# Kernel tuning notes

Hardware: AMD Instinct MI355X
Metric: run time of the kernel (lower is better)

## Reference

```python
import jax, jax.numpy as jnp
import numpy as np

N_HEAD = 16

def setup_inputs() -> dict:
    key = jax.random.key(0)
    k1, k2, k3 = jax.random.split(key, 3)
    B, T, C = 4, 2048, 1024
    x = jax.random.normal(k1, (B, T, C), dtype=jnp.float32)
    w_attn = jax.random.normal(k2, (C, 3 * C), dtype=jnp.float32) * (1.0 / np.sqrt(C))
    w_proj = jax.random.normal(k3, (C, C), dtype=jnp.float32) * (1.0 / np.sqrt(C))
    return {"x": x, "w_attn": w_attn, "w_proj": w_proj}

def reference(x, w_attn, w_proj):
    B, T, C = x.shape
    H = N_HEAD
    D = C // H
    qkv = x @ w_attn  # [B, T, 3C]
    q, k, v = jnp.split(qkv, 3, axis=2)
    # [B, H, T, D]
    q = q.reshape(B, T, H, D).transpose(0, 2, 1, 3)
    k = k.reshape(B, T, H, D).transpose(0, 2, 1, 3)
    v = v.reshape(B, T, H, D).transpose(0, 2, 1, 3)
    att = jnp.einsum('bhqd,bhkd->bhqk', q, k) * (1.0 / np.sqrt(D))
    causal = jnp.tril(jnp.ones((T, T), dtype=bool))
    att = jnp.where(causal[None, None, :, :], att, -jnp.inf)
    att = jax.nn.softmax(att, axis=-1)
    y = jnp.einsum('bhqk,bhkd->bhqd', att, v)  # [B, H, T, D]
    y = y.transpose(0, 2, 1, 3).reshape(B, T, C)
    return y @ w_proj
```

## Files before the change

kernel.cpp:

```cpp
#include <hip/hip_runtime.h>
#include <hip/hip_bf16.h>
#include <math.h>

#define B_   4
#define T_   2048
#define C_   1024
#define H_   16
#define D_   64
#define M_   (B_*T_)
#define N3   (3*C_)
#define KDIM C_

typedef __attribute__((ext_vector_type(8)))  short bf16x8;
typedef __attribute__((ext_vector_type(4)))  float f32x4;
typedef __attribute__((ext_vector_type(16))) float f32x16;
typedef __attribute__((ext_vector_type(4)))  unsigned int u32x4;

#define MFMA16(a,b,c) __builtin_amdgcn_mfma_f32_16x16x32_bf16(a,b,c,0,0,0)
#define MFMA32(a,b,c) __builtin_amdgcn_mfma_f32_32x32x16_bf16(a,b,c,0,0,0)

#define QSCALE 0.18033688011112042f

__device__ __forceinline__ unsigned short f2bf(float f) {
  union { float f; unsigned u; } a; a.f = f;
  unsigned r = a.u + 0x7fffu + ((a.u >> 16) & 1u);
  return (unsigned short)(r >> 16);
}

__device__ __forceinline__ unsigned cvtpk(float lo, float hi) {
  unsigned r;
  asm("v_cvt_pk_bf16_f32 %0, %1, %2" : "=v"(r) : "v"(lo), "v"(hi));
  return r;
}

__device__ __forceinline__ void gload16(const void* g, void* l) {
  __builtin_amdgcn_global_load_lds(
      (const __attribute__((address_space(1))) void*)g,
      (__attribute__((address_space(3))) void*)l, 16, 0, 0);
}

__global__ void cast_f32_bf16(const float* __restrict__ in,
                              unsigned short* __restrict__ out, int n) {
  int i = (blockIdx.x * 256 + threadIdx.x) * 4;
  if (i >= n) return;
  float4 v = *(const float4*)(in + i);
  ushort4 o;
  o.x = f2bf(v.x); o.y = f2bf(v.y); o.z = f2bf(v.z); o.w = f2bf(v.w);
  *(ushort4*)(out + i) = o;
}

__global__ void transpose_cast(const float* __restrict__ in,
                               unsigned short* __restrict__ out,
                               int R, int Ncols) {
  __shared__ float tile[32][33];
  int bc = blockIdx.x * 32;
  int br = blockIdx.y * 32;
  int tx = threadIdx.x, ty = threadIdx.y;
  #pragma unroll
  for (int i = ty; i < 32; i += 8)
    tile[i][tx] = in[(size_t)(br + i) * Ncols + bc + tx];
  __syncthreads();
  #pragma unroll
  for (int i = ty; i < 32; i += 8)
    out[(size_t)(bc + i) * R + br + tx] = f2bf(tile[tx][i]);
}

template<int MODE>
__global__ __launch_bounds__(256)
void gemm128(const unsigned short* __restrict__ A,
             const unsigned short* __restrict__ Bt,
             unsigned short* __restrict__ qo,
             unsigned short* __restrict__ ko,
             unsigned short* __restrict__ vto,
             float* __restrict__ outf) {
  __shared__ short Asl[128 * 64];
  __shared__ short Bsl[128 * 64];
  const int tid  = threadIdx.x;
  const int wid  = tid >> 6, lane = tid & 63;
  const int l15  = lane & 15, l4 = lane >> 4;
  const int tm   = blockIdx.y * 128;
  const int tn   = blockIdx.x * 128;
  const int wm   = (wid >> 1) * 64, wn = (wid & 1) * 64;

  f32x4 acc[4][4] = {};
  const int stoff = wid * 1024 + lane * 16;

  for (int kt = 0; kt < KDIM; kt += 64) {
    __syncthreads();
    #pragma unroll
    for (int ro = 0; ro < 4; ++ro) {
      int off = ro * 4096 + stoff;
      int row = off >> 7;
      int ce  = (off & 127) >> 1;
      gload16(A  + (size_t)(tm + row) * KDIM + kt + ce,
              (char*)Asl + ro * 4096 + wid * 1024);
      gload16(Bt + (size_t)(tn + row) * KDIM + kt + ce,
              (char*)Bsl + ro * 4096 + wid * 1024);
    }
    __syncthreads();

    #pragma unroll
    for (int ks = 0; ks < 2; ++ks) {
      bf16x8 af[4], bfr[4];
      #pragma unroll
      for (int i = 0; i < 4; ++i) {
        af[i]  = *(const bf16x8*)&Asl[(wm + i*16 + l15) * 64 + ks*32 + l4*8];
        bfr[i] = *(const bf16x8*)&Bsl[(wn + i*16 + l15) * 64 + ks*32 + l4*8];
      }
      #pragma unroll
      for (int mi = 0; mi < 4; ++mi)
        #pragma unroll
        for (int ni = 0; ni < 4; ++ni)
          acc[mi][ni] = MFMA16(af[mi], bfr[ni], acc[mi][ni]);
    }
  }

  #pragma unroll
  for (int mi = 0; mi < 4; ++mi) {
    #pragma unroll
    for (int ni = 0; ni < 4; ++ni) {
      #pragma unroll
      for (int r = 0; r < 4; ++r) {
        int m = tm + wm + mi*16 + l4*4 + r;
        int n = tn + wn + ni*16 + l15;
        float val = acc[mi][ni][r];
        if (MODE == 0) {
          int b = m >> 11, t = m & (T_ - 1);
          int which = n >> 10, n1 = n & (C_ - 1);
          int h = n1 >> 6, d = n1 & 63;
          size_t bh = (size_t)(b * H_ + h);
          if (which == 0)      qo[(bh * T_ + t) * D_ + d] = f2bf(val * QSCALE);
          else if (which == 1) ko[(bh * T_ + t) * D_ + d] = f2bf(val);
          else                 vto[(bh * D_ + d) * T_ + t] = f2bf(val);
        } else {
          outf[(size_t)m * C_ + n] = val;
        }
      }
    }
  }
}

__global__ __launch_bounds__(256)
void attn32(const unsigned short* __restrict__ Q,
            const unsigned short* __restrict__ K,
            const unsigned short* __restrict__ Vt,
            unsigned short* __restrict__ Y) {
  const int bh   = blockIdx.x;
  const int y    = blockIdx.y;
  const int lane = threadIdx.x & 63, w = threadIdx.x >> 6;
  const int l31  = lane & 31, hi = lane >> 5;
  const int b    = bh >> 4, h = bh & 15;

  const int qsub = (w < 2) ? (2*y + w) : (63 - 2*y - (w & 1));
  const int q0   = qsub * 32;

  const unsigned short* Qp = Q  + (size_t)bh * T_ * D_;
  const unsigned short* Kp = K  + (size_t)bh * T_ * D_;
  const unsigned short* Vp = Vt + (size_t)bh * D_ * T_;

  bf16x8 qf[4];
  #pragma unroll
  for (int c = 0; c < 4; ++c)
    qf[c] = *(const bf16x8*)&Qp[(size_t)(q0 + l31) * D_ + c*16 + hi*8];

  f32x16 acc[2] = {};
  float m_q = -INFINITY, l_q = 0.f;

  const int nt = (q0 + 31) / 64 + 1;

  bf16x8 kfc[2][4];
  #pragma unroll
  for (int kb = 0; kb < 2; ++kb)
    #pragma unroll
    for (int c = 0; c < 4; ++c)
      kfc[kb][c] = *(const bf16x8*)&Kp[(size_t)(kb*32 + l31) * D_ + c*16 + hi*8];

  for (int kt = 0; kt < nt; ++kt) {
    const int k0 = kt * 64;

    f32x16 s2[2] = {};
    __builtin_amdgcn_s_setprio(1);
    #pragma unroll
    for (int c = 0; c < 4; ++c) s2[0] = MFMA32(kfc[0][c], qf[c], s2[0]);
    #pragma unroll
    for (int c = 0; c < 4; ++c) s2[1] = MFMA32(kfc[1][c], qf[c], s2[1]);
    __builtin_amdgcn_s_setprio(0);

    if (kt + 1 < nt) {
      const int k1 = k0 + 64;
      #pragma unroll
      for (int kb = 0; kb < 2; ++kb)
        #pragma unroll
        for (int c = 0; c < 4; ++c)
          kfc[kb][c] = *(const bf16x8*)&Kp[(size_t)(k1 + kb*32 + l31) * D_ + c*16 + hi*8];
    }

    if (kt == nt - 1) {
      #pragma unroll
      for (int kb = 0; kb < 2; ++kb)
        #pragma unroll
        for (int r = 0; r < 16; ++r) {
          int krow = k0 + kb*32 + (r&3) + 8*(r>>2) + 4*hi;
          if (krow > q0 + l31) s2[kb][r] = -INFINITY;
        }
    }

    float tmax = s2[0][0];
    #pragma unroll
    for (int kb = 0; kb < 2; ++kb)
      #pragma unroll
      for (int r = 0; r < 16; ++r) tmax = fmaxf(tmax, s2[kb][r]);

    if (!__all(tmax <= m_q + 8.0f)) {
      float tm2 = fmaxf(tmax, __shfl_xor(tmax, 32, 64));
      float mn  = fmaxf(m_q, tm2);
      float scale = exp2f(m_q - mn);
      m_q = mn;
      l_q *= scale;
      #pragma unroll
      for (int r = 0; r < 16; ++r) { acc[0][r] *= scale; acc[1][r] *= scale; }
    }

    float rsum = 0.f;
    #pragma unroll
    for (int kb = 0; kb < 2; ++kb)
      #pragma unroll
      for (int r = 0; r < 16; ++r) {
        float pe = exp2f(s2[kb][r] - m_q);
        s2[kb][r] = pe;
        rsum += pe;
      }
    rsum += __shfl_xor(rsum, 32, 64);
    l_q += rsum;

    u32x4 pb[4];
    #pragma unroll
    for (int kb = 0; kb < 2; ++kb)
      #pragma unroll
      for (int ss = 0; ss < 2; ++ss)
        #pragma unroll
        for (int b2 = 0; b2 < 2; ++b2) {
          unsigned ce = cvtpk(s2[kb][8*ss     + 2*b2], s2[kb][8*ss     + 2*b2 + 1]);
          unsigned co = cvtpk(s2[kb][8*ss + 4 + 2*b2], s2[kb][8*ss + 4 + 2*b2 + 1]);
          auto rr = __builtin_amdgcn_permlane32_swap(ce, co, false, false);
          pb[kb*2 + ss][b2]     = rr[0];
          pb[kb*2 + ss][2 + b2] = rr[1];
        }

    #pragma unroll
    for (int dt = 0; dt < 2; ++dt) {
      bf16x8 va[4];
      #pragma unroll
      for (int s = 0; s < 4; ++s)
        va[s] = *(const bf16x8*)&Vp[(size_t)(dt*32 + l31) * T_ + k0 + s*16 + hi*8];
      __builtin_amdgcn_s_setprio(1);
      #pragma unroll
      for (int s = 0; s < 4; ++s)
        acc[dt] = MFMA32(va[s], __builtin_bit_cast(bf16x8, pb[s]), acc[dt]);
      __builtin_amdgcn_s_setprio(0);
    }
  }

  float inv = 1.0f / l_q;
  const int t = q0 + l31;
  unsigned short* Yrow = Y + ((size_t)b * T_ + t) * C_ + h * D_;
  #pragma unroll
  for (int dt = 0; dt < 2; ++dt)
    #pragma unroll
    for (int rg = 0; rg < 4; ++rg) {
      uint2 wv;
      wv.x = cvtpk(acc[dt][rg*4 + 0] * inv, acc[dt][rg*4 + 1] * inv);
      wv.y = cvtpk(acc[dt][rg*4 + 2] * inv, acc[dt][rg*4 + 3] * inv);
      *(uint2*)(Yrow + dt*32 + rg*8 + hi*4) = wv;
    }
}

extern "C" void kernel_launch(void* const* d_in, const int* in_sizes, int n_in,
                              void* d_out, int out_size, void* d_ws, size_t ws_size,
                              hipStream_t stream) {
  const float* x      = (const float*)d_in[0];
  const float* w_attn = (const float*)d_in[1];
  const float* w_proj = (const float*)d_in[2];
  float* out = (float*)d_out;

  char* ws = (char*)d_ws;
  size_t off = 0;
  auto alloc = [&](size_t bytes) {
    char* p = ws + off; off += (bytes + 255) & ~(size_t)255; return p;
  };
  unsigned short* xb  = (unsigned short*)alloc((size_t)M_ * C_ * 2);
  unsigned short* wat = (unsigned short*)alloc((size_t)N3 * KDIM * 2);
  unsigned short* wpt = (unsigned short*)alloc((size_t)C_ * C_ * 2);
  unsigned short* qb  = (unsigned short*)alloc((size_t)M_ * C_ * 2);
  unsigned short* kb  = (unsigned short*)alloc((size_t)M_ * C_ * 2);
  unsigned short* vtb = (unsigned short*)alloc((size_t)M_ * C_ * 2);
  unsigned short* yb  = (unsigned short*)alloc((size_t)M_ * C_ * 2);

  cast_f32_bf16<<<dim3(M_ * C_ / 1024), dim3(256), 0, stream>>>(x, xb, M_ * C_);
  transpose_cast<<<dim3(N3 / 32, KDIM / 32), dim3(32, 8), 0, stream>>>(w_attn, wat, KDIM, N3);
  transpose_cast<<<dim3(C_ / 32, C_ / 32), dim3(32, 8), 0, stream>>>(w_proj, wpt, C_, C_);

  gemm128<0><<<dim3(N3 / 128, M_ / 128), dim3(256), 0, stream>>>(xb, wat, qb, kb, vtb, nullptr);
  attn32<<<dim3(B_ * H_, 16), dim3(256), 0, stream>>>(qb, kb, vtb, yb);
  gemm128<1><<<dim3(C_ / 128, M_ / 128), dim3(256), 0, stream>>>(yb, wpt, nullptr, nullptr, nullptr, out);
}
```

Baseline: 357.0 us.

## Coalesce V-transpose epilogue via LDS and rebalance causal attention work per wave

The QKV GEMM epilogue for the V third now stages the tile through swizzled shared memory and writes the transposed V in 16-byte coalesced chunks, replacing strided 2-byte scattered stores. The attention kernel gives each wave a pair of query sub-tiles (j and 63-j), processed one after the other, so every wave does equal causal work. Inside the loop the V loads are issued earlier and the next K prefetch is interleaved between the two PV MFMA groups to hide latency. The costs are an extra LDS round trip with barriers in the GEMM and a longer serial per-wave loop in attention. The nt bound also changes to q0/64+1.

```diff
diff --git a/kernel.cpp b/kernel.cpp
--- a/kernel.cpp
+++ b/kernel.cpp
@@ -73,8 +73,9 @@
              unsigned short* __restrict__ ko,
              unsigned short* __restrict__ vto,
              float* __restrict__ outf) {
-  __shared__ short Asl[128 * 64];
-  __shared__ short Bsl[128 * 64];
+  __shared__ short smem[2 * 128 * 64];
+  short* Asl = smem;
+  short* Bsl = smem + 128 * 64;
   const int tid  = threadIdx.x;
   const int wid  = tid >> 6, lane = tid & 63;
   const int l15  = lane & 15, l4 = lane >> 4;
@@ -115,27 +116,58 @@
     }
   }
 
-  #pragma unroll
-  for (int mi = 0; mi < 4; ++mi) {
-    #pragma unroll
-    for (int ni = 0; ni < 4; ++ni) {
-      #pragma unroll
-      for (int r = 0; r < 4; ++r) {
-        int m = tm + wm + mi*16 + l4*4 + r;
-        int n = tn + wn + ni*16 + l15;
-        float val = acc[mi][ni][r];
-        if (MODE == 0) {
+  if (MODE == 1) {
+    #pragma unroll
+    for (int mi = 0; mi < 4; ++mi)
+      #pragma unroll
+      for (int ni = 0; ni < 4; ++ni)
+        #pragma unroll
+        for (int r = 0; r < 4; ++r) {
+          int m = tm + wm + mi*16 + l4*4 + r;
+          int n = tn + wn + ni*16 + l15;
+          outf[(size_t)m * C_ + n] = acc[mi][ni][r];
+        }
+  } else if (tn < 2 * C_) {
+    #pragma unroll
+    for (int mi = 0; mi < 4; ++mi)
+      #pragma unroll
+      for (int ni = 0; ni < 4; ++ni)
+        #pragma unroll
+        for (int r = 0; r < 4; ++r) {
+          int m = tm + wm + mi*16 + l4*4 + r;
+          int n = tn + wn + ni*16 + l15;
+          float val = acc[mi][ni][r];
           int b = m >> 11, t = m & (T_ - 1);
           int which = n >> 10, n1 = n & (C_ - 1);
           int h = n1 >> 6, d = n1 & 63;
           size_t bh = (size_t)(b * H_ + h);
-          if (which == 0)      qo[(bh * T_ + t) * D_ + d] = f2bf(val * QSCALE);
-          else if (which == 1) ko[(bh * T_ + t) * D_ + d] = f2bf(val);
-          else                 vto[(bh * D_ + d) * T_ + t] = f2bf(val);
-        } else {
-          outf[(size_t)m * C_ + n] = val;
+          if (which == 0) qo[(bh * T_ + t) * D_ + d] = f2bf(val * QSCALE);
+          else            ko[(bh * T_ + t) * D_ + d] = f2bf(val);
         }
-      }
+  } else {
+    __syncthreads();
+    #pragma unroll
+    for (int mi = 0; mi < 4; ++mi)
+      #pragma unroll
+      for (int ni = 0; ni < 4; ++ni) {
+        int nl = wn + ni*16 + l15;
+        int ml = wm + mi*16 + l4*4;
+        ushort4 wv;
+        wv.x = f2bf(acc[mi][ni][0]); wv.y = f2bf(acc[mi][ni][1]);
+        wv.z = f2bf(acc[mi][ni][2]); wv.w = f2bf(acc[mi][ni][3]);
+        *(ushort4*)&smem[nl * 128 + (ml ^ ((nl & 7) << 3))] = wv;
+      }
+    __syncthreads();
+    const int b0 = tm >> 11, t0 = tm & (T_ - 1);
+    const int h0 = (tn - 2 * C_) >> 6;
+    #pragma unroll
+    for (int it = 0; it < 8; ++it) {
+      int idx = it * 256 + tid;
+      int row = idx >> 4;
+      int m0  = (idx & 15) * 8;
+      bf16x8 v = *(const bf16x8*)&smem[row * 128 + (m0 ^ ((row & 7) << 3))];
+      size_t dst = ((size_t)((b0 * H_ + h0 + (row >> 6)) * D_ + (row & 63))) * T_ + t0 + m0;
+      *(bf16x8*)&vto[dst] = v;
     }
   }
 }
@@ -146,133 +178,142 @@
             const unsigned short* __restrict__ Vt,
             unsigned short* __restrict__ Y) {
   const int bh   = blockIdx.x;
-  const int y    = blockIdx.y;
+  const int yblk = blockIdx.y;
   const int lane = threadIdx.x & 63, w = threadIdx.x >> 6;
   const int l31  = lane & 31, hi = lane >> 5;
   const int b    = bh >> 4, h = bh & 15;
-
-  const int qsub = (w < 2) ? (2*y + w) : (63 - 2*y - (w & 1));
-  const int q0   = qsub * 32;
+  const int j0   = yblk * 4 + w;
 
   const unsigned short* Qp = Q  + (size_t)bh * T_ * D_;
   const unsigned short* Kp = K  + (size_t)bh * T_ * D_;
   const unsigned short* Vp = Vt + (size_t)bh * D_ * T_;
 
-  bf16x8 qf[4];
-  #pragma unroll
-  for (int c = 0; c < 4; ++c)
-    qf[c] = *(const bf16x8*)&Qp[(size_t)(q0 + l31) * D_ + c*16 + hi*8];
-
-  f32x16 acc[2] = {};
-  float m_q = -INFINITY, l_q = 0.f;
-
-  const int nt = (q0 + 31) / 64 + 1;
-
-  bf16x8 kfc[2][4];
-  #pragma unroll
-  for (int kb = 0; kb < 2; ++kb)
+  for (int half = 0; half < 2; ++half) {
+    const int qsub = half ? (63 - j0) : j0;
+    const int q0   = qsub * 32;
+
+    bf16x8 qf[4];
     #pragma unroll
     for (int c = 0; c < 4; ++c)
-      kfc[kb][c] = *(const bf16x8*)&Kp[(size_t)(kb*32 + l31) * D_ + c*16 + hi*8];
-
-  for (int kt = 0; kt < nt; ++kt) {
-    const int k0 = kt * 64;
-
-    f32x16 s2[2] = {};
-    __builtin_amdgcn_s_setprio(1);
-    #pragma unroll
-    for (int c = 0; c < 4; ++c) s2[0] = MFMA32(kfc[0][c], qf[c], s2[0]);
-    #pragma unroll
-    for (int c = 0; c < 4; ++c) s2[1] = MFMA32(kfc[1][c], qf[c], s2[1]);
-    __builtin_amdgcn_s_setprio(0);
-
-    if (kt + 1 < nt) {
-      const int k1 = k0 + 64;
+      qf[c] = *(const bf16x8*)&Qp[(size_t)(q0 + l31) * D_ + c*16 + hi*8];
+
+    f32x16 acc[2] = {};
+    float m_q = -INFINITY, l_q = 0.f;
+
+    const int nt = q0 / 64 + 1;
+
+    bf16x8 kfc[2][4];
+    #pragma unroll
+    for (int kb = 0; kb < 2; ++kb)
+      #pragma unroll
+      for (int c = 0; c < 4; ++c)
+        kfc[kb][c] = *(const bf16x8*)&Kp[(size_t)(kb*32 + l31) * D_ + c*16 + hi*8];
+
+    for (int kt = 0; kt < nt; ++kt) {
+      const int k0 = kt * 64;
+
+      f32x16 s2[2] = {};
+      __builtin_amdgcn_s_setprio(1);
+      #pragma unroll
+      for (int c = 0; c < 4; ++c) s2[0] = MFMA32(kfc[0][c], qf[c], s2[0]);
+      #pragma unroll
+      for (int c = 0; c < 4; ++c) s2[1] = MFMA32(kfc[1][c], qf[c], s2[1]);
+      __builtin_amdgcn_s_setprio(0);
+
+      bf16x8 va[2][4];
+      #pragma unroll
+      for (int dt = 0; dt < 2; ++dt)
+        #pragma unroll
+        for (int s = 0; s < 4; ++s)
+          va[dt][s] = *(const bf16x8*)&Vp[(size_t)(dt*32 + l31) * T_ + k0 + s*16 + hi*8];
+
+      if (kt == nt - 1) {
+        #pragma unroll
+        for (int kb = 0; kb < 2; ++kb)
+          #pragma unroll
+          for (int r = 0; r < 16; ++r) {
+            int krow = k0 + kb*32 + (r&3) + 8*(r>>2) + 4*hi;
+            if (krow > q0 + l31) s2[kb][r] = -INFINITY;
+          }
+      }
+
+      float tmax = s2[0][0];
       #pragma unroll
       for (int kb = 0; kb < 2; ++kb)
         #pragma unroll
-        for (int c = 0; c < 4; ++c)
-          kfc[kb][c] = *(const bf16x8*)&Kp[(size_t)(k1 + kb*32 + l31) * D_ + c*16 + hi*8];
-    }
-
-    if (kt == nt - 1) {
+        for (int r = 0; r < 16; ++r) tmax = fmaxf(tmax, s2[kb][r]);
+
+      if (!__all(tmax <= m_q + 8.0f)) {
+        float tm2 = fmaxf(tmax, __shfl_xor(tmax, 32, 64));
+        float mn  = fmaxf(m_q, tm2);
+        float scale = exp2f(m_q - mn);
+        m_q = mn;
+        l_q *= scale;
+        #pragma unroll
+        for (int r = 0; r < 16; ++r) { acc[0][r] *= scale; acc[1][r] *= scale; }
+      }
+
+      float rsum = 0.f;
       #pragma unroll
       for (int kb = 0; kb < 2; ++kb)
         #pragma unroll
         for (int r = 0; r < 16; ++r) {
-          int krow = k0 + kb*32 + (r&3) + 8*(r>>2) + 4*hi;
-          if (krow > q0 + l31) s2[kb][r] = -INFINITY;
+          float pe = exp2f(s2[kb][r] - m_q);
+          s2[kb][r] = pe;
+          rsum += pe;
         }
-    }
-
-    float tmax = s2[0][0];
-    #pragma unroll
-    for (int kb = 0; kb < 2; ++kb)
-      #pragma unroll
-      for (int r = 0; r < 16; ++r) tmax = fmaxf(tmax, s2[kb][r]);
-
-    if (!__all(tmax <= m_q + 8.0f)) {
-      float tm2 = fmaxf(tmax, __shfl_xor(tmax, 32, 64));
-      float mn  = fmaxf(m_q, tm2);
-      float scale = exp2f(m_q - mn);
-      m_q = mn;
-      l_q *= scale;
-      #pragma unroll
-      for (int r = 0; r < 16; ++r) { acc[0][r] *= scale; acc[1][r] *= scale; }
-    }
-
-    float rsum = 0.f;
-    #pragma unroll
-    for (int kb = 0; kb < 2; ++kb)
-      #pragma unroll
-      for (int r = 0; r < 16; ++r) {
-        float pe = exp2f(s2[kb][r] - m_q);
-        s2[kb][r] = pe;
-        rsum += pe;
-      }
-    rsum += __shfl_xor(rsum, 32, 64);
-    l_q += rsum;
-
-    u32x4 pb[4];
-    #pragma unroll
-    for (int kb = 0; kb < 2; ++kb)
-      #pragma unroll
-      for (int ss = 0; ss < 2; ++ss)
-        #pragma unroll
-        for (int b2 = 0; b2 < 2; ++b2) {
-          unsigned ce = cvtpk(s2[kb][8*ss     + 2*b2], s2[kb][8*ss     + 2*b2 + 1]);
-          unsigned co = cvtpk(s2[kb][8*ss + 4 + 2*b2], s2[kb][8*ss + 4 + 2*b2 + 1]);
-          auto rr = __builtin_amdgcn_permlane32_swap(ce, co, false, false);
-          pb[kb*2 + ss][b2]     = rr[0];
-          pb[kb*2 + ss][2 + b2] = rr[1];
-        }
-
-    #pragma unroll
-    for (int dt = 0; dt < 2; ++dt) {
-      bf16x8 va[4];
+      rsum += __shfl_xor(rsum, 32, 64);
+      l_q += rsum;
+
+      u32x4 pb[4];
+      #pragma unroll
+      for (int kb = 0; kb < 2; ++kb)
+        #pragma unroll
+        for (int ss = 0; ss < 2; ++ss)
+          #pragma unroll
+          for (int b2 = 0; b2 < 2; ++b2) {
+            unsigned ce = cvtpk(s2[kb][8*ss     + 2*b2], s2[kb][8*ss     + 2*b2 + 1]);
+            unsigned co = cvtpk(s2[kb][8*ss + 4 + 2*b2], s2[kb][8*ss + 4 + 2*b2 + 1]);
+            auto rr = __builtin_amdgcn_permlane32_swap(ce, co, false, false);
+            pb[kb*2 + ss][b2]     = rr[0];
+            pb[kb*2 + ss][2 + b2] = rr[1];
+          }
+
+      __builtin_amdgcn_s_setprio(1);
       #pragma unroll
       for (int s = 0; s < 4; ++s)
-        va[s] = *(const bf16x8*)&Vp[(size_t)(dt*32 + l31) * T_ + k0 + s*16 + hi*8];
+        acc[0] = MFMA32(va[0][s], __builtin_bit_cast(bf16x8, pb[s]), acc[0]);
+      __builtin_amdgcn_s_setprio(0);
+
+      if (kt + 1 < nt) {
+        const int k1 = k0 + 64;
+        #pragma unroll
+        for (int kb = 0; kb < 2; ++kb)
+          #pragma unroll
+          for (int c = 0; c < 4; ++c)
+            kfc[kb][c] = *(const bf16x8*)&Kp[(size_t)(k1 + kb*32 + l31) * D_ + c*16 + hi*8];
+      }
+
       __builtin_amdgcn_s_setprio(1);
       #pragma unroll
       for (int s = 0; s < 4; ++s)
-        acc[dt] = MFMA32(va[s], __builtin_bit_cast(bf16x8, pb[s]), acc[dt]);
+        acc[1] = MFMA32(va[1][s], __builtin_bit_cast(bf16x8, pb[s]), acc[1]);
       __builtin_amdgcn_s_setprio(0);
     }
+
+    float inv = 1.0f / l_q;
+    const int t = q0 + l31;
+    unsigned short* Yrow = Y + ((size_t)b * T_ + t) * C_ + h * D_;
+    #pragma unroll
+    for (int dt = 0; dt < 2; ++dt)
+      #pragma unroll
+      for (int rg = 0; rg < 4; ++rg) {
+        uint2 wv;
+        wv.x = cvtpk(acc[dt][rg*4 + 0] * inv, acc[dt][rg*4 + 1] * inv);
+        wv.y = cvtpk(acc[dt][rg*4 + 2] * inv, acc[dt][rg*4 + 3] * inv);
+        *(uint2*)(Yrow + dt*32 + rg*8 + hi*4) = wv;
+      }
   }
-
-  float inv = 1.0f / l_q;
-  const int t = q0 + l31;
-  unsigned short* Yrow = Y + ((size_t)b * T_ + t) * C_ + h * D_;
-  #pragma unroll
-  for (int dt = 0; dt < 2; ++dt)
-    #pragma unroll
-    for (int rg = 0; rg < 4; ++rg) {
-      uint2 wv;
-      wv.x = cvtpk(acc[dt][rg*4 + 0] * inv, acc[dt][rg*4 + 1] * inv);
-      wv.y = cvtpk(acc[dt][rg*4 + 2] * inv, acc[dt][rg*4 + 3] * inv);
-      *(uint2*)(Yrow + dt*32 + rg*8 + hi*4) = wv;
-    }
 }
 
 extern "C" void kernel_launch(void* const* d_in, const int* in_sizes, int n_in,
```

Result: slower. 445.4 us (+24.8%).
